# Kernel optimization log

Hardware: AMD Instinct MI355X
Metric: run time of the kernel (lower is better)

Reference implementation:

```python
import jax, jax.numpy as jnp
import numpy as np

DIM = 256; HEADS = 8; DEPTH = 2; DFF = 128
T = 64      # timesteps (transformer batch dim for s_transformer)
N = 2048    # total agents
S = 256     # number of segments (scenes)
L = 8       # agents per segment (N = S*L)
HD = DIM // HEADS
LN_EPS = 1e-5


def _ln(x, w, b):
    m = x.mean(-1, keepdims=True)
    v = x.var(-1, keepdims=True)
    return (x - m) / jnp.sqrt(v + LN_EPS) * w + b


def _mha(x, qkvw, qkvb, ow, ob):
    B, Sq, D = x.shape
    qkv = x @ qkvw.T + qkvb                      # [B,Sq,3D]
    q, k, v = jnp.split(qkv, 3, axis=-1)
    def sp(t):
        return t.reshape(B, Sq, HEADS, HD).transpose(0, 2, 1, 3)
    q, k, v = sp(q), sp(k), sp(v)
    a = jax.nn.softmax(jnp.einsum('bhqd,bhkd->bhqk', q, k) * (1.0 / (HD ** 0.5)))
    o = jnp.einsum('bhqk,bhkd->bhqd', a, v).transpose(0, 2, 1, 3).reshape(B, Sq, D)
    return o @ ow.T + ob


def _layer(x, qkvw, qkvb, ow, ob, l1w, l1b, l2w, l2b, ln1w, ln1b, ln2w, ln2b):
    # PyTorch TransformerEncoderLayer, post-norm, relu FFN
    x = _ln(x + _mha(x, qkvw, qkvb, ow, ob), ln1w, ln1b)
    h = jax.nn.relu(x @ l1w.T + l1b) @ l2w.T + l2b
    return _ln(x + h, ln2w, ln2b)


def _encoder(x, qkvw, qkvb, ow, ob, l1w, l1b, l2w, l2b, ln1w, ln1b, ln2w, ln2b):
    for i in range(DEPTH):
        x = _layer(x, qkvw[i], qkvb[i], ow[i], ob[i], l1w[i], l1b[i],
                   l2w[i], l2b[i], ln1w[i], ln1b[i], ln2w[i], ln2b[i])
    return x


def setup_inputs() -> dict:
    key = jax.random.key(0)
    ks = iter(jax.random.split(key, 64))
    def rn(shape, scale=0.05):
        return jax.random.normal(next(ks), shape, dtype=jnp.float32) * scale
    inp = {}
    inp['moveinfo'] = jax.random.normal(next(ks), (N, T, 2), dtype=jnp.float32)
    starts = jnp.arange(S, dtype=jnp.int32) * L
    inp['seq_start_end'] = jnp.stack([starts, starts + L], axis=1)  # [S,2]
    inp['w_in'] = rn((DIM, 2)); inp['b_in'] = rn((DIM,))
    for p in ('s', 't'):
        inp[p + '_qkvw'] = rn((DEPTH, 3 * DIM, DIM)); inp[p + '_qkvb'] = rn((DEPTH, 3 * DIM))
        inp[p + '_ow'] = rn((DEPTH, DIM, DIM)); inp[p + '_ob'] = rn((DEPTH, DIM))
        inp[p + '_l1w'] = rn((DEPTH, DFF, DIM)); inp[p + '_l1b'] = rn((DEPTH, DFF))
        inp[p + '_l2w'] = rn((DEPTH, DIM, DFF)); inp[p + '_l2b'] = rn((DEPTH, DIM))
        inp[p + '_ln1w'] = jnp.ones((DEPTH, DIM)); inp[p + '_ln1b'] = jnp.zeros((DEPTH, DIM))
        inp[p + '_ln2w'] = jnp.ones((DEPTH, DIM)); inp[p + '_ln2b'] = jnp.zeros((DEPTH, DIM))
    return inp


def reference(moveinfo, seq_start_end, w_in, b_in,
              s_qkvw, s_qkvb, s_ow, s_ob, s_l1w, s_l1b, s_l2w, s_l2b,
              s_ln1w, s_ln1b, s_ln2w, s_ln2b,
              t_qkvw, t_qkvb, t_ow, t_ob, t_l1w, t_l1b, t_l2w, t_l2b,
              t_ln1w, t_ln1b, t_ln2w, t_ln2b):
    # to_dim: Linear(2, dim) + exact GELU
    s_in = jax.nn.gelu(jnp.einsum('ntc,dc->ntd', moveinfo, w_in) + b_in, approximate=False)
    s_in = s_in.transpose(1, 0, 2)                       # [T, N, D]
    # gather equal-length segments: ragged loop batched as one attention call
    idx = seq_start_end[:, 0][:, None] + jnp.arange(L)   # [S, L]
    seg = s_in[:, idx, :].reshape(T * S, L, DIM)         # [T*S, L, D]
    cls = jnp.full((T * S, 1, DIM), 1e-5, dtype=s_in.dtype)
    x = jnp.concatenate([cls, seg], axis=1)              # [T*S, 1+L, D]
    x = _encoder(x, s_qkvw, s_qkvb, s_ow, s_ob, s_l1w, s_l1b, s_l2w, s_l2b,
                 s_ln1w, s_ln1b, s_ln2w, s_ln2b)
    t_in = x[:, 0, :].reshape(T, S, DIM).transpose(1, 0, 2)  # [S, T, D]
    out = _encoder(t_in, t_qkvw, t_qkvb, t_ow, t_ob, t_l1w, t_l1b, t_l2w, t_l2b,
                   t_ln1w, t_ln1b, t_ln2w, t_ln2b)
    return out
```

## Files before the change

kernel.cpp:

```cpp
#include <hip/hip_runtime.h>
#include <hip/hip_bf16.h>
#include <math.h>

typedef __bf16 bf16_t;
typedef float floatx4 __attribute__((ext_vector_type(4)));
typedef bf16_t bf16x8 __attribute__((ext_vector_type(8)));

typedef __attribute__((address_space(1))) void g_void;
typedef __attribute__((address_space(3))) void lds_void;

__device__ __forceinline__ void ldg_lds16(const bf16_t* g, bf16_t* l) {
    __builtin_amdgcn_global_load_lds((g_void*)g, (lds_void*)l, 16, 0, 0);
}

__device__ __forceinline__ void unpack4(uint2 r, float* o) {
    o[0] = __uint_as_float((r.x & 0xffffu) << 16); o[1] = __uint_as_float(r.x & 0xffff0000u);
    o[2] = __uint_as_float((r.y & 0xffffu) << 16); o[3] = __uint_as_float(r.y & 0xffff0000u);
}

__global__ void cvt_weights(const float* __restrict__ sqkvw, const float* __restrict__ sow,
                            const float* __restrict__ sl1w,  const float* __restrict__ sl2w,
                            const float* __restrict__ tqkvw, const float* __restrict__ tow,
                            const float* __restrict__ tl1w,  const float* __restrict__ tl2w,
                            bf16_t* __restrict__ dst) {
    int i = blockIdx.x * 256 + threadIdx.x;
    float v;
    if      (i <  393216) v = sqkvw[i];
    else if (i <  524288) v = sow  [i -  393216];
    else if (i <  589824) v = sl1w [i -  524288];
    else if (i <  655360) v = sl2w [i -  589824];
    else if (i < 1048576) v = tqkvw[i -  655360];
    else if (i < 1179648) v = tow  [i - 1048576];
    else if (i < 1245184) v = tl1w [i - 1179648];
    else                  v = tl2w [i - 1245184];
    dst[i] = (bf16_t)v;
}

__global__ void embed_k(const float* __restrict__ mv, const float* __restrict__ w_in,
                        const float* __restrict__ b_in, bf16_t* __restrict__ x, int b0) {
    int blk = blockIdx.x; int d = threadIdx.x;
    int tok = blk % 9; int lb = blk / 9;
    size_t oidx = (size_t)blk * 256 + d;
    if (tok == 0) { x[oidx] = (bf16_t)1e-5f; return; }
    int bb = b0 + lb; int t = bb >> 8; int s = bb & 255;
    int n = s * 8 + (tok - 1);
    float m0 = mv[((size_t)n * 64 + t) * 2];
    float m1 = mv[((size_t)n * 64 + t) * 2 + 1];
    float v = m0 * w_in[2 * d] + m1 * w_in[2 * d + 1] + b_in[d];
    v = 0.5f * v * (1.0f + erff(v * 0.70710678118654752f));
    x[oidx] = (bf16_t)v;
}

__global__ void cls_k(const bf16_t* __restrict__ x, bf16_t* __restrict__ txb,
                      float* __restrict__ txf, int b0) {
    int lb = blockIdx.x; int d = threadIdx.x;
    int bb = b0 + lb; int t = bb >> 8; int s = bb & 255;
    bf16_t v = x[(size_t)lb * 2304 + d];
    size_t di = ((size_t)(s * 64 + t)) * 256 + d;
    txb[di] = v;
    txf[di] = (float)v;
}

__global__ __launch_bounds__(256) void gemm_bt(const bf16_t* __restrict__ A,
                                               const bf16_t* __restrict__ W,
                                               const float* __restrict__ bias,
                                               bf16_t* __restrict__ C,
                                               int M, int N, int K, int relu) {
    __shared__ __align__(16) bf16_t As[8192];
    __shared__ __align__(16) bf16_t Ws[8192];
    int MT = M >> 7, NT = N >> 7;
    int g = blockIdx.x;
    int m_t, n_t;
    if ((MT & 7) == 0) {
        int x = g & 7, q = g >> 3;
        m_t = (q / NT) * 8 + x;
        n_t = q % NT;
    } else {
        m_t = g / NT; n_t = g % NT;
    }
    int tid = threadIdx.x;
    int lane = tid & 63;
    int wave = tid >> 6;
    int m0 = m_t * 128;
    int n0 = n_t * 128;
    int wm = (wave & 1) * 64;
    int wn = (wave >> 1) * 64;
    int arow = tid >> 2;
    int acol = (tid & 3) * 8;
    int fm = lane & 15;
    int fq = lane >> 4;

    floatx4 acc[4][4] = {};

    const bf16_t* Ag = A + (size_t)(m0 + arow) * K + acol;
    const bf16_t* Wg = W + (size_t)(n0 + arow) * K + acol;

    for (int k0 = 0; k0 < K; k0 += 64) {
        __syncthreads();
        ldg_lds16(Ag + k0,                       &As[tid * 8]);
        ldg_lds16(Ag + k0 + (size_t)64 * K,      &As[2048 + tid * 8]);
        ldg_lds16(Ag + k0 + 32,                  &As[4096 + tid * 8]);
        ldg_lds16(Ag + k0 + 32 + (size_t)64 * K, &As[6144 + tid * 8]);
        ldg_lds16(Wg + k0,                       &Ws[tid * 8]);
        ldg_lds16(Wg + k0 + (size_t)64 * K,      &Ws[2048 + tid * 8]);
        ldg_lds16(Wg + k0 + 32,                  &Ws[4096 + tid * 8]);
        ldg_lds16(Wg + k0 + 32 + (size_t)64 * K, &Ws[6144 + tid * 8]);
        __syncthreads();

#pragma unroll
        for (int sl = 0; sl < 2; sl++) {
            int base = sl * 4096;
            bf16x8 af[4], wf[4];
#pragma unroll
            for (int mi = 0; mi < 4; mi++)
                af[mi] = *(const bf16x8*)&As[base + (wm + mi * 16 + fm) * 32 + fq * 8];
#pragma unroll
            for (int ni = 0; ni < 4; ni++)
                wf[ni] = *(const bf16x8*)&Ws[base + (wn + ni * 16 + fm) * 32 + fq * 8];
#pragma unroll
            for (int mi = 0; mi < 4; mi++)
#pragma unroll
                for (int ni = 0; ni < 4; ni++)
                    acc[mi][ni] = __builtin_amdgcn_mfma_f32_16x16x32_bf16(wf[ni], af[mi], acc[mi][ni], 0, 0, 0);
        }
    }

#pragma unroll
    for (int mi = 0; mi < 4; mi++) {
        int row = m0 + wm + mi * 16 + fm;
#pragma unroll
        for (int ni = 0; ni < 4; ni++) {
            int colb = n0 + wn + ni * 16 + fq * 4;
            float4 b4 = *(const float4*)(bias + colb);
            float v0 = acc[mi][ni][0] + b4.x;
            float v1 = acc[mi][ni][1] + b4.y;
            float v2 = acc[mi][ni][2] + b4.z;
            float v3 = acc[mi][ni][3] + b4.w;
            if (relu) {
                v0 = fmaxf(v0, 0.f); v1 = fmaxf(v1, 0.f);
                v2 = fmaxf(v2, 0.f); v3 = fmaxf(v3, 0.f);
            }
            bf16_t t4[4] = {(bf16_t)v0, (bf16_t)v1, (bf16_t)v2, (bf16_t)v3};
            *(uint2*)(C + (size_t)row * N + colb) = *(uint2*)t4;
        }
    }
}

__global__ __launch_bounds__(256) void attn9_k(const bf16_t* __restrict__ qkv,
                                               bf16_t* __restrict__ ao) {
    __shared__ __align__(16) bf16_t sb[27648];
    int b = blockIdx.x; int tid = threadIdx.x;
    const uint4* src = (const uint4*)(qkv + (size_t)b * 27648);
    uint4* dstl = (uint4*)sb;
    for (int c = tid; c < 3456; c += 256) dstl[c] = src[c];
    __syncthreads();
    for (int p = tid; p < 288; p += 256) {
        int s = p / 72; int rem = p - s * 72; int h = rem / 9; int i = rem - h * 9;
        const bf16_t* B = sb + s * 6912;
        const bf16_t* qp = B + i * 768 + h * 32;
        float qf[32];
#pragma unroll
        for (int c = 0; c < 4; c++) {
            bf16x8 t8 = *(const bf16x8*)(qp + c * 8);
#pragma unroll
            for (int e = 0; e < 8; e++) qf[c * 8 + e] = (float)t8[e];
        }
        float sc[9]; float mx = -1e30f;
#pragma unroll
        for (int j = 0; j < 9; j++) {
            const bf16_t* kp = B + j * 768 + 256 + h * 32;
            float d = 0.f;
#pragma unroll
            for (int c = 0; c < 4; c++) {
                bf16x8 t8 = *(const bf16x8*)(kp + c * 8);
#pragma unroll
                for (int e = 0; e < 8; e++) d += qf[c * 8 + e] * (float)t8[e];
            }
            d *= 0.17677669529663687f;
            sc[j] = d; mx = fmaxf(mx, d);
        }
        float den = 0.f;
#pragma unroll
        for (int j = 0; j < 9; j++) { sc[j] = __expf(sc[j] - mx); den += sc[j]; }
        float inv = 1.0f / den;
        float of[32] = {};
#pragma unroll
        for (int j = 0; j < 9; j++) {
            const bf16_t* vp = B + j * 768 + 512 + h * 32;
            float w = sc[j];
#pragma unroll
            for (int c = 0; c < 4; c++) {
                bf16x8 t8 = *(const bf16x8*)(vp + c * 8);
#pragma unroll
                for (int e = 0; e < 8; e++) of[c * 8 + e] += w * (float)t8[e];
            }
        }
        bf16_t* dst = ao + ((size_t)(b * 4 + s) * 9 + i) * 256 + h * 32;
#pragma unroll
        for (int c = 0; c < 4; c++) {
            bf16x8 o8;
#pragma unroll
            for (int e = 0; e < 8; e++) o8[e] = (bf16_t)(of[c * 8 + e] * inv);
            *(bf16x8*)(dst + c * 8) = o8;
        }
    }
}

__global__ __launch_bounds__(256) void attn64_k(const bf16_t* __restrict__ qkv,
                                                bf16_t* __restrict__ ao) {
    __shared__ __align__(16) float kk[64 * 36];
    __shared__ __align__(16) float vv[64 * 36];
    __shared__ __align__(16) float pp[64 * 64];
    __shared__ float mloc[4 * 64];
    __shared__ float sloc[4 * 64];
    int s = blockIdx.x >> 3, h = blockIdx.x & 7;
    int t = threadIdx.x;
    int i = t & 63;
    int wq = t >> 6;

    {
        int r = t >> 2, c = t & 3;
        const bf16_t* kb = qkv + ((size_t)(s * 64 + r)) * 768 + h * 32 + 256 + c * 8;
        bf16x8 k8 = *(const bf16x8*)kb;
        bf16x8 v8 = *(const bf16x8*)(kb + 256);
        float* kd = &kk[r * 36 + c * 8];
        float* vd = &vv[r * 36 + c * 8];
#pragma unroll
        for (int e = 0; e < 8; e++) { kd[e] = (float)k8[e]; vd[e] = (float)v8[e]; }
    }
    const bf16_t* qb = qkv + ((size_t)(s * 64 + i)) * 768 + h * 32;
    float qf[32];
#pragma unroll
    for (int c = 0; c < 4; c++) {
        bf16x8 t8 = *(const bf16x8*)(qb + c * 8);
#pragma unroll
        for (int e = 0; e < 8; e++) qf[c * 8 + e] = (float)t8[e];
    }
    __syncthreads();

    float sc[16]; float mx = -1e30f;
#pragma unroll
    for (int jj = 0; jj < 16; jj++) {
        int j = wq * 16 + jj;
        const float* kr = &kk[j * 36];
        float d = 0.f;
#pragma unroll
        for (int c = 0; c < 8; c++) {
            float4 k4 = *(const float4*)(kr + c * 4);
            d += qf[c*4+0]*k4.x + qf[c*4+1]*k4.y + qf[c*4+2]*k4.z + qf[c*4+3]*k4.w;
        }
        d *= 0.17677669529663687f;
        sc[jj] = d; mx = fmaxf(mx, d);
    }
    float se = 0.f;
#pragma unroll
    for (int jj = 0; jj < 16; jj++) se += __expf(sc[jj] - mx);
    mloc[wq * 64 + i] = mx;
    sloc[wq * 64 + i] = se;
    __syncthreads();

    float m0 = mloc[i], m1 = mloc[64 + i], m2 = mloc[128 + i], m3 = mloc[192 + i];
    float gm = fmaxf(fmaxf(m0, m1), fmaxf(m2, m3));
    float D = sloc[i] * __expf(m0 - gm) + sloc[64 + i] * __expf(m1 - gm)
            + sloc[128 + i] * __expf(m2 - gm) + sloc[192 + i] * __expf(m3 - gm);

#pragma unroll
    for (int jj = 0; jj < 16; jj++)
        pp[(wq * 16 + jj) * 64 + i] = __expf(sc[jj] - gm);
    __syncthreads();

    float of[8] = {};
    for (int j = 0; j < 64; j++) {
        float w = pp[j * 64 + i];
        const float* vr = &vv[j * 36 + wq * 8];
        float4 va = *(const float4*)vr;
        float4 vb = *(const float4*)(vr + 4);
        of[0] += w * va.x; of[1] += w * va.y; of[2] += w * va.z; of[3] += w * va.w;
        of[4] += w * vb.x; of[5] += w * vb.y; of[6] += w * vb.z; of[7] += w * vb.w;
    }
    float invD = 1.0f / D;
    bf16_t o8[8];
#pragma unroll
    for (int e = 0; e < 8; e++) o8[e] = (bf16_t)(of[e] * invD);
    *(uint4*)(ao + ((size_t)(s * 64 + i)) * 256 + h * 32 + wq * 8) = *(uint4*)o8;
}

__global__ __launch_bounds__(256) void resln_k(const bf16_t* __restrict__ xin_bf,
                                               const float* __restrict__ xin_f,
                                               const bf16_t* __restrict__ add,
                                               const float* __restrict__ w,
                                               const float* __restrict__ b,
                                               bf16_t* __restrict__ out_bf,
                                               float* __restrict__ out_f) {
    int row = blockIdx.x * 4 + (threadIdx.x >> 6);
    int lane = threadIdx.x & 63;
    size_t base = (size_t)row * 256 + lane * 4;
    float xv[4], av[4], v[4];
    if (xin_f) {
        float4 t = *(const float4*)(xin_f + base);
        xv[0] = t.x; xv[1] = t.y; xv[2] = t.z; xv[3] = t.w;
    } else {
        unpack4(*(const uint2*)(xin_bf + base), xv);
    }
    unpack4(*(const uint2*)(add + base), av);
    float s = 0.f, ss = 0.f;
#pragma unroll
    for (int i = 0; i < 4; i++) { v[i] = xv[i] + av[i]; s += v[i]; ss += v[i] * v[i]; }
#pragma unroll
    for (int off = 32; off > 0; off >>= 1) {
        s += __shfl_xor(s, off, 64);
        ss += __shfl_xor(ss, off, 64);
    }
    float mean = s * (1.f / 256.f);
    float var = ss * (1.f / 256.f) - mean * mean;
    float inv = rsqrtf(var + 1e-5f);
    float o[4];
#pragma unroll
    for (int i = 0; i < 4; i++)
        o[i] = (v[i] - mean) * inv * w[lane * 4 + i] + b[lane * 4 + i];
    if (out_bf) {
        bf16_t tmp[4] = {(bf16_t)o[0], (bf16_t)o[1], (bf16_t)o[2], (bf16_t)o[3]};
        *(uint2*)(out_bf + base) = *(uint2*)tmp;
    }
    if (out_f) {
        float4 t; t.x = o[0]; t.y = o[1]; t.z = o[2]; t.w = o[3];
        *(float4*)(out_f + base) = t;
    }
}

extern "C" void kernel_launch(void* const* d_in, const int* in_sizes, int n_in,
                              void* d_out, int out_size, void* d_ws, size_t ws_size,
                              hipStream_t stream) {
    const float* mv   = (const float*)d_in[0];
    const float* w_in = (const float*)d_in[2];
    const float* b_in = (const float*)d_in[3];
    const float* sp[12]; const float* tp[12];
    for (int i = 0; i < 12; i++) { sp[i] = (const float*)d_in[4 + i]; tp[i] = (const float*)d_in[16 + i]; }

    bf16_t* wbf = (bf16_t*)d_ws;
    bf16_t* txb = wbf + 1310720;
    float*  txf = (float*)(txb + 4194304);
    bf16_t* pool = (bf16_t*)(txf + 4194304);

    long long headB = 2621440LL + 8388608LL + 16777216LL;
    long long cand[5] = {16384, 8192, 4096, 2048, 1024};
    int BC = 1024;
    for (int c = 0; c < 5; c++) {
        long long poolB = cand[c] * 11520LL * 2;
        if (poolB < 33554432LL) poolB = 33554432LL;
        if ((size_t)(headB + poolB) <= ws_size) { BC = (int)cand[c]; break; }
    }

    cvt_weights<<<5120, 256, 0, stream>>>(sp[0], sp[2], sp[4], sp[6], tp[0], tp[2], tp[4], tp[6], wbf);

    const int M = BC * 9;
    const int MTb = M / 128;
    bf16_t* xc    = pool;
    bf16_t* qkvb_ = pool + (long long)BC * 2304;
    bf16_t* aob   = qkvb_ + (long long)BC * 6912;
    bf16_t* pob   = qkvb_;
    bf16_t* hb    = qkvb_;
    bf16_t* f2b   = qkvb_ + (long long)M * 128;

    for (int b0 = 0; b0 < 16384; b0 += BC) {
        embed_k<<<dim3(M), 256, 0, stream>>>(mv, w_in, b_in, xc, b0);
        for (int l = 0; l < 2; l++) {
            const bf16_t* wq = wbf + 0      + l * 196608;
            const bf16_t* wo = wbf + 393216 + l * 65536;
            const bf16_t* w1 = wbf + 524288 + l * 32768;
            const bf16_t* w2 = wbf + 589824 + l * 32768;
            gemm_bt<<<dim3(MTb * 6), 256, 0, stream>>>(xc, wq, sp[1] + l * 768, qkvb_, M, 768, 256, 0);
            attn9_k<<<dim3(BC / 4), 256, 0, stream>>>(qkvb_, aob);
            gemm_bt<<<dim3(MTb * 2), 256, 0, stream>>>(aob, wo, sp[3] + l * 256, pob, M, 256, 256, 0);
            resln_k<<<dim3(M / 4), 256, 0, stream>>>(xc, (const float*)nullptr, pob,
                                                     sp[8] + l * 256, sp[9] + l * 256,
                                                     xc, (float*)nullptr);
            gemm_bt<<<dim3(MTb * 1), 256, 0, stream>>>(xc, w1, sp[5] + l * 128, hb, M, 128, 256, 1);
            gemm_bt<<<dim3(MTb * 2), 256, 0, stream>>>(hb, w2, sp[7] + l * 256, f2b, M, 256, 128, 0);
            resln_k<<<dim3(M / 4), 256, 0, stream>>>(xc, (const float*)nullptr, f2b,
                                                     sp[10] + l * 256, sp[11] + l * 256,
                                                     xc, (float*)nullptr);
        }
        cls_k<<<dim3(BC), 256, 0, stream>>>(xc, txb, txf, b0);
    }

    const int Mt = 16384;
    bf16_t* tqkv = pool;
    bf16_t* tao  = pool + 12582912;
    bf16_t* tpo  = pool;
    bf16_t* tth  = pool + 4194304;
    bf16_t* tf2  = pool + 4194304 + 2097152;
    for (int l = 0; l < 2; l++) {
        gemm_bt<<<dim3(128 * 6), 256, 0, stream>>>(txb, wbf + 655360 + l * 196608, tp[1] + l * 768,
                                                   tqkv, Mt, 768, 256, 0);
        attn64_k<<<dim3(2048), 256, 0, stream>>>(tqkv, tao);
        gemm_bt<<<dim3(128 * 2), 256, 0, stream>>>(tao, wbf + 1048576 + l * 65536, tp[3] + l * 256,
                                                   tpo, Mt, 256, 256, 0);
        resln_k<<<dim3(4096), 256, 0, stream>>>((const bf16_t*)nullptr, txf, tpo,
                                                tp[8] + l * 256, tp[9] + l * 256,
                                                txb, txf);
        gemm_bt<<<dim3(128 * 1), 256, 0, stream>>>(txb, wbf + 1179648 + l * 32768, tp[5] + l * 128,
                                                   tth, Mt, 128, 256, 1);
        gemm_bt<<<dim3(128 * 2), 256, 0, stream>>>(tth, wbf + 1245184 + l * 32768, tp[7] + l * 256,
                                                   tf2, Mt, 256, 128, 0);
        if (l == 0)
            resln_k<<<dim3(4096), 256, 0, stream>>>((const bf16_t*)nullptr, txf, tf2,
                                                    tp[10] + l * 256, tp[11] + l * 256,
                                                    txb, txf);
        else
            resln_k<<<dim3(4096), 256, 0, stream>>>((const bf16_t*)nullptr, txf, tf2,
                                                    tp[10] + l * 256, tp[11] + l * 256,
                                                    (bf16_t*)nullptr, (float*)d_out);
    }
}
```

Measured before the change: 1.203 ms.

## Fuse residual+LayerNorm into projection GEMM and fuse full FFN with LayerNorm

Replaces the out-projection GEMM plus separate residual-LayerNorm kernel with one kernel whose 128x256 tile covers full rows, so the LN is computed in the epilogue via a cross-wave reduction in shared memory. The FFN's two GEMMs, ReLU, residual and LN are merged into one kernel that keeps the hidden activations in LDS and reads w2 directly from global. This removes intermediate tensor round trips and several launches per layer. In exchange the grid is much smaller (M/128 blocks, e.g. 128 blocks in the temporal encoder), which may underfill the GPU, and the kernels use more registers and LDS.

New measurement: 1.265 ms. +5.1%, slower.

```diff
diff --git a/kernel.cpp b/kernel.cpp
--- a/kernel.cpp
+++ b/kernel.cpp
@@ -146,6 +146,222 @@
     }
 }
 
+__device__ __forceinline__ void epilogue_resln(
+    floatx4 (&acc)[4][8], int m0, int wm, int wn, int fm, int fq, int wave,
+    const float* __restrict__ bias, const bf16_t* __restrict__ res_bf,
+    const float* __restrict__ res_f, const float* __restrict__ lnw,
+    const float* __restrict__ lnb, bf16_t* __restrict__ out_bf,
+    float* __restrict__ out_f, float (*rs)[128], float (*rss)[128]) {
+    float s[4] = {0.f, 0.f, 0.f, 0.f}, ss[4] = {0.f, 0.f, 0.f, 0.f};
+#pragma unroll
+    for (int mi = 0; mi < 4; mi++) {
+        size_t row = (size_t)(m0 + wm + mi * 16 + fm);
+#pragma unroll
+        for (int ni = 0; ni < 8; ni++) {
+            int col = wn + ni * 16 + fq * 4;
+            float4 b4 = *(const float4*)(bias + col);
+            float r4[4];
+            if (res_f) {
+                float4 t = *(const float4*)(res_f + row * 256 + col);
+                r4[0] = t.x; r4[1] = t.y; r4[2] = t.z; r4[3] = t.w;
+            } else {
+                unpack4(*(const uint2*)(res_bf + row * 256 + col), r4);
+            }
+            float v0 = acc[mi][ni][0] + b4.x + r4[0];
+            float v1 = acc[mi][ni][1] + b4.y + r4[1];
+            float v2 = acc[mi][ni][2] + b4.z + r4[2];
+            float v3 = acc[mi][ni][3] + b4.w + r4[3];
+            acc[mi][ni][0] = v0; acc[mi][ni][1] = v1;
+            acc[mi][ni][2] = v2; acc[mi][ni][3] = v3;
+            s[mi] += v0 + v1 + v2 + v3;
+            ss[mi] += v0 * v0 + v1 * v1 + v2 * v2 + v3 * v3;
+        }
+    }
+#pragma unroll
+    for (int mi = 0; mi < 4; mi++) {
+        s[mi]  += __shfl_xor(s[mi], 16);  s[mi]  += __shfl_xor(s[mi], 32);
+        ss[mi] += __shfl_xor(ss[mi], 16); ss[mi] += __shfl_xor(ss[mi], 32);
+    }
+    if (fq == 0) {
+#pragma unroll
+        for (int mi = 0; mi < 4; mi++) {
+            rs [wave >> 1][wm + mi * 16 + fm] = s[mi];
+            rss[wave >> 1][wm + mi * 16 + fm] = ss[mi];
+        }
+    }
+    __syncthreads();
+#pragma unroll
+    for (int mi = 0; mi < 4; mi++) {
+        int lrow = wm + mi * 16 + fm;
+        size_t row = (size_t)(m0 + lrow);
+        float mean = (rs[0][lrow] + rs[1][lrow]) * (1.f / 256.f);
+        float var  = (rss[0][lrow] + rss[1][lrow]) * (1.f / 256.f) - mean * mean;
+        float inv = rsqrtf(var + 1e-5f);
+#pragma unroll
+        for (int ni = 0; ni < 8; ni++) {
+            int col = wn + ni * 16 + fq * 4;
+            float4 w4 = *(const float4*)(lnw + col);
+            float4 bl = *(const float4*)(lnb + col);
+            float o0 = (acc[mi][ni][0] - mean) * inv * w4.x + bl.x;
+            float o1 = (acc[mi][ni][1] - mean) * inv * w4.y + bl.y;
+            float o2 = (acc[mi][ni][2] - mean) * inv * w4.z + bl.z;
+            float o3 = (acc[mi][ni][3] - mean) * inv * w4.w + bl.w;
+            if (out_bf) {
+                bf16_t t4[4] = {(bf16_t)o0, (bf16_t)o1, (bf16_t)o2, (bf16_t)o3};
+                *(uint2*)(out_bf + row * 256 + col) = *(uint2*)t4;
+            }
+            if (out_f) {
+                float4 t; t.x = o0; t.y = o1; t.z = o2; t.w = o3;
+                *(float4*)(out_f + row * 256 + col) = t;
+            }
+        }
+    }
+}
+
+__global__ __launch_bounds__(256) void gemm_proj_ln(const bf16_t* __restrict__ A,
+                                                    const bf16_t* __restrict__ W,
+                                                    const float* __restrict__ bias,
+                                                    const bf16_t* __restrict__ res_bf,
+                                                    const float* __restrict__ res_f,
+                                                    const float* __restrict__ lnw,
+                                                    const float* __restrict__ lnb,
+                                                    bf16_t* __restrict__ out_bf,
+                                                    float* __restrict__ out_f) {
+    __shared__ __align__(16) bf16_t As[8192];
+    __shared__ __align__(16) bf16_t Ws[16384];
+    __shared__ float rs[2][128], rss[2][128];
+    int tid = threadIdx.x;
+    int lane = tid & 63, wave = tid >> 6;
+    int m0 = blockIdx.x * 128;
+    int wm = (wave & 1) * 64;
+    int wn = (wave >> 1) * 128;
+    int arow = tid >> 2, acol = (tid & 3) * 8;
+    int fm = lane & 15, fq = lane >> 4;
+    floatx4 acc[4][8] = {};
+    const bf16_t* Ag = A + (size_t)(m0 + arow) * 256 + acol;
+    const bf16_t* Wg = W + (size_t)arow * 256 + acol;
+    for (int k0 = 0; k0 < 256; k0 += 64) {
+        __syncthreads();
+        ldg_lds16(Ag + k0,              &As[tid * 8]);
+        ldg_lds16(Ag + k0 + 16384,      &As[2048 + tid * 8]);
+        ldg_lds16(Ag + k0 + 32,         &As[4096 + tid * 8]);
+        ldg_lds16(Ag + k0 + 32 + 16384, &As[6144 + tid * 8]);
+        ldg_lds16(Wg + k0,              &Ws[tid * 8]);
+        ldg_lds16(Wg + k0 + 16384,      &Ws[2048 + tid * 8]);
+        ldg_lds16(Wg + k0 + 32768,      &Ws[4096 + tid * 8]);
+        ldg_lds16(Wg + k0 + 49152,      &Ws[6144 + tid * 8]);
+        ldg_lds16(Wg + k0 + 32,         &Ws[8192 + tid * 8]);
+        ldg_lds16(Wg + k0 + 32 + 16384, &Ws[10240 + tid * 8]);
+        ldg_lds16(Wg + k0 + 32 + 32768, &Ws[12288 + tid * 8]);
+        ldg_lds16(Wg + k0 + 32 + 49152, &Ws[14336 + tid * 8]);
+        __syncthreads();
+#pragma unroll
+        for (int sl = 0; sl < 2; sl++) {
+            bf16x8 af[4], wf[8];
+#pragma unroll
+            for (int mi = 0; mi < 4; mi++)
+                af[mi] = *(const bf16x8*)&As[sl * 4096 + (wm + mi * 16 + fm) * 32 + fq * 8];
+#pragma unroll
+            for (int ni = 0; ni < 8; ni++)
+                wf[ni] = *(const bf16x8*)&Ws[sl * 8192 + (wn + ni * 16 + fm) * 32 + fq * 8];
+#pragma unroll
+            for (int mi = 0; mi < 4; mi++)
+#pragma unroll
+                for (int ni = 0; ni < 8; ni++)
+                    acc[mi][ni] = __builtin_amdgcn_mfma_f32_16x16x32_bf16(wf[ni], af[mi], acc[mi][ni], 0, 0, 0);
+        }
+    }
+    epilogue_resln(acc, m0, wm, wn, fm, fq, wave, bias, res_bf, res_f,
+                   lnw, lnb, out_bf, out_f, rs, rss);
+}
+
+__global__ __launch_bounds__(256) void gemm_ffn_ln(const bf16_t* __restrict__ X,
+                                                   const bf16_t* __restrict__ w1,
+                                                   const float* __restrict__ b1,
+                                                   const bf16_t* __restrict__ w2,
+                                                   const float* __restrict__ b2,
+                                                   const float* __restrict__ lnw,
+                                                   const float* __restrict__ lnb,
+                                                   const float* __restrict__ res_f,
+                                                   bf16_t* __restrict__ out_bf,
+                                                   float* __restrict__ out_f) {
+    __shared__ __align__(16) bf16_t As[8192];
+    __shared__ __align__(16) bf16_t Ws[8192];
+    __shared__ __align__(16) bf16_t Hs[20480];
+    __shared__ float rs[2][128], rss[2][128];
+    int tid = threadIdx.x, lane = tid & 63, wave = tid >> 6;
+    int m0 = blockIdx.x * 128;
+    int wm = (wave & 1) * 64;
+    int wn1 = (wave >> 1) * 64;
+    int wn2 = (wave >> 1) * 128;
+    int arow = tid >> 2, acol = (tid & 3) * 8;
+    int fm = lane & 15, fq = lane >> 4;
+    floatx4 acc[4][4] = {};
+    const bf16_t* Ag = X + (size_t)(m0 + arow) * 256 + acol;
+    const bf16_t* Wg = w1 + (size_t)arow * 256 + acol;
+    for (int k0 = 0; k0 < 256; k0 += 64) {
+        __syncthreads();
+        ldg_lds16(Ag + k0,              &As[tid * 8]);
+        ldg_lds16(Ag + k0 + 16384,      &As[2048 + tid * 8]);
+        ldg_lds16(Ag + k0 + 32,         &As[4096 + tid * 8]);
+        ldg_lds16(Ag + k0 + 32 + 16384, &As[6144 + tid * 8]);
+        ldg_lds16(Wg + k0,              &Ws[tid * 8]);
+        ldg_lds16(Wg + k0 + 16384,      &Ws[2048 + tid * 8]);
+        ldg_lds16(Wg + k0 + 32,         &Ws[4096 + tid * 8]);
+        ldg_lds16(Wg + k0 + 32 + 16384, &Ws[6144 + tid * 8]);
+        __syncthreads();
+#pragma unroll
+        for (int sl = 0; sl < 2; sl++) {
+            int base = sl * 4096;
+            bf16x8 af[4], wf[4];
+#pragma unroll
+            for (int mi = 0; mi < 4; mi++)
+                af[mi] = *(const bf16x8*)&As[base + (wm + mi * 16 + fm) * 32 + fq * 8];
+#pragma unroll
+            for (int ni = 0; ni < 4; ni++)
+                wf[ni] = *(const bf16x8*)&Ws[base + (wn1 + ni * 16 + fm) * 32 + fq * 8];
+#pragma unroll
+            for (int mi = 0; mi < 4; mi++)
+#pragma unroll
+                for (int ni = 0; ni < 4; ni++)
+                    acc[mi][ni] = __builtin_amdgcn_mfma_f32_16x16x32_bf16(wf[ni], af[mi], acc[mi][ni], 0, 0, 0);
+        }
+    }
+#pragma unroll
+    for (int mi = 0; mi < 4; mi++) {
+        int row = wm + mi * 16 + fm;
+#pragma unroll
+        for (int ni = 0; ni < 4; ni++) {
+            int c = wn1 + ni * 16 + fq * 4;
+            float4 b4 = *(const float4*)(b1 + c);
+            bf16_t t4[4];
+            t4[0] = (bf16_t)fmaxf(acc[mi][ni][0] + b4.x, 0.f);
+            t4[1] = (bf16_t)fmaxf(acc[mi][ni][1] + b4.y, 0.f);
+            t4[2] = (bf16_t)fmaxf(acc[mi][ni][2] + b4.z, 0.f);
+            t4[3] = (bf16_t)fmaxf(acc[mi][ni][3] + b4.w, 0.f);
+            *(uint2*)&Hs[(c >> 5) * 5120 + row * 40 + (c & 31)] = *(uint2*)t4;
+        }
+    }
+    __syncthreads();
+    floatx4 acc2[4][8] = {};
+#pragma unroll
+    for (int ks = 0; ks < 4; ks++) {
+        bf16x8 af2[4];
+#pragma unroll
+        for (int mi = 0; mi < 4; mi++)
+            af2[mi] = *(const bf16x8*)&Hs[ks * 5120 + (wm + mi * 16 + fm) * 40 + fq * 8];
+#pragma unroll
+        for (int ni = 0; ni < 8; ni++) {
+            bf16x8 wf2 = *(const bf16x8*)(w2 + (size_t)(wn2 + ni * 16 + fm) * 128 + ks * 32 + fq * 8);
+#pragma unroll
+            for (int mi = 0; mi < 4; mi++)
+                acc2[mi][ni] = __builtin_amdgcn_mfma_f32_16x16x32_bf16(wf2, af2[mi], acc2[mi][ni], 0, 0, 0);
+        }
+    }
+    epilogue_resln(acc2, m0, wm, wn2, fm, fq, wave, b2, X, res_f,
+                   lnw, lnb, out_bf, out_f, rs, rss);
+}
+
 __global__ __launch_bounds__(256) void attn9_k(const bf16_t* __restrict__ qkv,
                                                bf16_t* __restrict__ ao) {
     __shared__ __align__(16) bf16_t sb[27648];
@@ -285,49 +501,6 @@
     *(uint4*)(ao + ((size_t)(s * 64 + i)) * 256 + h * 32 + wq * 8) = *(uint4*)o8;
 }
 
-__global__ __launch_bounds__(256) void resln_k(const bf16_t* __restrict__ xin_bf,
-                                               const float* __restrict__ xin_f,
-                                               const bf16_t* __restrict__ add,
-                                               const float* __restrict__ w,
-                                               const float* __restrict__ b,
-                                               bf16_t* __restrict__ out_bf,
-                                               float* __restrict__ out_f) {
-    int row = blockIdx.x * 4 + (threadIdx.x >> 6);
-    int lane = threadIdx.x & 63;
-    size_t base = (size_t)row * 256 + lane * 4;
-    float xv[4], av[4], v[4];
-    if (xin_f) {
-        float4 t = *(const float4*)(xin_f + base);
-        xv[0] = t.x; xv[1] = t.y; xv[2] = t.z; xv[3] = t.w;
-    } else {
-        unpack4(*(const uint2*)(xin_bf + base), xv);
-    }
-    unpack4(*(const uint2*)(add + base), av);
-    float s = 0.f, ss = 0.f;
-#pragma unroll
-    for (int i = 0; i < 4; i++) { v[i] = xv[i] + av[i]; s += v[i]; ss += v[i] * v[i]; }
-#pragma unroll
-    for (int off = 32; off > 0; off >>= 1) {
-        s += __shfl_xor(s, off, 64);
-        ss += __shfl_xor(ss, off, 64);
-    }
-    float mean = s * (1.f / 256.f);
-    float var = ss * (1.f / 256.f) - mean * mean;
-    float inv = rsqrtf(var + 1e-5f);
-    float o[4];
-#pragma unroll
-    for (int i = 0; i < 4; i++)
-        o[i] = (v[i] - mean) * inv * w[lane * 4 + i] + b[lane * 4 + i];
-    if (out_bf) {
-        bf16_t tmp[4] = {(bf16_t)o[0], (bf16_t)o[1], (bf16_t)o[2], (bf16_t)o[3]};
-        *(uint2*)(out_bf + base) = *(uint2*)tmp;
-    }
-    if (out_f) {
-        float4 t; t.x = o[0]; t.y = o[1]; t.z = o[2]; t.w = o[3];
-        *(float4*)(out_f + base) = t;
-    }
-}
-
 extern "C" void kernel_launch(void* const* d_in, const int* in_sizes, int n_in,
                               void* d_out, int out_size, void* d_ws, size_t ws_size,
                               hipStream_t stream) {
@@ -358,9 +531,6 @@
     bf16_t* xc    = pool;
     bf16_t* qkvb_ = pool + (long long)BC * 2304;
     bf16_t* aob   = qkvb_ + (long long)BC * 6912;
-    bf16_t* pob   = qkvb_;
-    bf16_t* hb    = qkvb_;
-    bf16_t* f2b   = qkvb_ + (long long)M * 128;
 
     for (int b0 = 0; b0 < 16384; b0 += BC) {
         embed_k<<<dim3(M), 256, 0, stream>>>(mv, w_in, b_in, xc, b0);
@@ -371,45 +541,34 @@
             const bf16_t* w2 = wbf + 589824 + l * 32768;
             gemm_bt<<<dim3(MTb * 6), 256, 0, stream>>>(xc, wq, sp[1] + l * 768, qkvb_, M, 768, 256, 0);
             attn9_k<<<dim3(BC / 4), 256, 0, stream>>>(qkvb_, aob);
-            gemm_bt<<<dim3(MTb * 2), 256, 0, stream>>>(aob, wo, sp[3] + l * 256, pob, M, 256, 256, 0);
-            resln_k<<<dim3(M / 4), 256, 0, stream>>>(xc, (const float*)nullptr, pob,
-                                                     sp[8] + l * 256, sp[9] + l * 256,
-                                                     xc, (float*)nullptr);
-            gemm_bt<<<dim3(MTb * 1), 256, 0, stream>>>(xc, w1, sp[5] + l * 128, hb, M, 128, 256, 1);
-            gemm_bt<<<dim3(MTb * 2), 256, 0, stream>>>(hb, w2, sp[7] + l * 256, f2b, M, 256, 128, 0);
-            resln_k<<<dim3(M / 4), 256, 0, stream>>>(xc, (const float*)nullptr, f2b,
-                                                     sp[10] + l * 256, sp[11] + l * 256,
-                                                     xc, (float*)nullptr);
+            gemm_proj_ln<<<dim3(MTb), 256, 0, stream>>>(aob, wo, sp[3] + l * 256,
+                                                        xc, (const float*)nullptr,
+                                                        sp[8] + l * 256, sp[9] + l * 256,
+                                                        xc, (float*)nullptr);
+            gemm_ffn_ln<<<dim3(MTb), 256, 0, stream>>>(xc, w1, sp[5] + l * 128,
+                                                       w2, sp[7] + l * 256,
+                                                       sp[10] + l * 256, sp[11] + l * 256,
+                                                       (const float*)nullptr,
+                                                       xc, (float*)nullptr);
         }
         cls_k<<<dim3(BC), 256, 0, stream>>>(xc, txb, txf, b0);
     }
 
-    const int Mt = 16384;
     bf16_t* tqkv = pool;
     bf16_t* tao  = pool + 12582912;
-    bf16_t* tpo  = pool;
-    bf16_t* tth  = pool + 4194304;
-    bf16_t* tf2  = pool + 4194304 + 2097152;
     for (int l = 0; l < 2; l++) {
         gemm_bt<<<dim3(128 * 6), 256, 0, stream>>>(txb, wbf + 655360 + l * 196608, tp[1] + l * 768,
-                                                   tqkv, Mt, 768, 256, 0);
+                                                   tqkv, 16384, 768, 256, 0);
         attn64_k<<<dim3(2048), 256, 0, stream>>>(tqkv, tao);
-        gemm_bt<<<dim3(128 * 2), 256, 0, stream>>>(tao, wbf + 1048576 + l * 65536, tp[3] + l * 256,
-                                                   tpo, Mt, 256, 256, 0);
-        resln_k<<<dim3(4096), 256, 0, stream>>>((const bf16_t*)nullptr, txf, tpo,
-                                                tp[8] + l * 256, tp[9] + l * 256,
-                                                txb, txf);
-        gemm_bt<<<dim3(128 * 1), 256, 0, stream>>>(txb, wbf + 1179648 + l * 32768, tp[5] + l * 128,
-                                                   tth, Mt, 128, 256, 1);
-        gemm_bt<<<dim3(128 * 2), 256, 0, stream>>>(tth, wbf + 1245184 + l * 32768, tp[7] + l * 256,
-                                                   tf2, Mt, 256, 128, 0);
-        if (l == 0)
-            resln_k<<<dim3(4096), 256, 0, stream>>>((const bf16_t*)nullptr, txf, tf2,
-                                                    tp[10] + l * 256, tp[11] + l * 256,
+        gemm_proj_ln<<<dim3(128), 256, 0, stream>>>(tao, wbf + 1048576 + l * 65536, tp[3] + l * 256,
+                                                    (const bf16_t*)nullptr, txf,
+                                                    tp[8] + l * 256, tp[9] + l * 256,
                                                     txb, txf);
-        else
-            resln_k<<<dim3(4096), 256, 0, stream>>>((const bf16_t*)nullptr, txf, tf2,
-                                                    tp[10] + l * 256, tp[11] + l * 256,
-                                                    (bf16_t*)nullptr, (float*)d_out);
-    }
-}
+        gemm_ffn_ln<<<dim3(128), 256, 0, stream>>>(txb, wbf + 1179648 + l * 32768, tp[5] + l * 128,
+                                                   wbf + 1245184 + l * 32768, tp[7] + l * 256,
+                                                   tp[10] + l * 256, tp[11] + l * 256,
+                                                   txf,
+                                                   (l == 0) ? txb : (bf16_t*)nullptr,
+                                                   (l == 0) ? txf : (float*)d_out);
+    }
+}
```
